# Performance work log

Measured on AMD Instinct MI355X. Metric: run time of the kernel, lower is better.

## Reference

```python
import jax, jax.numpy as jnp
import numpy as np

WINDOW = 5
PAD = WINDOW // 2


def _extract_patches(x):
    # x: (B,C,H,W) -> patches (B,C,K*K,H,W) with reflect padding, matching
    # F.pad(mode='reflect') + F.unfold(window, padding=0).
    B, C, H, W = x.shape
    xp = jnp.pad(x, ((0, 0), (0, 0), (PAD, PAD), (PAD, PAD)), mode='reflect')
    patches = jnp.stack(
        [xp[:, :, i:i + H, j:j + W] for i in range(WINDOW) for j in range(WINDOW)],
        axis=2,
    )
    return patches


def setup_inputs() -> dict:
    key = jax.random.key(0)
    k1, k2, k3 = jax.random.split(key, 3)
    x = jax.random.normal(k1, (4, 32, 256, 256), dtype=jnp.float32)
    mix = jax.random.normal(k2, (1, 32, 1, 1), dtype=jnp.float32)
    beta_raw = jax.random.normal(k3, (), dtype=jnp.float32)
    return {"x": x, "mix": mix, "beta_raw": beta_raw}


def reference(x, mix, beta_raw):
    patches = _extract_patches(x)  # (B,C,25,H,W)

    # Max filter (= max_pool2d over reflect-padded input, stride 1)
    max_out = jnp.max(patches, axis=2)

    # Soft (differentiable) median filter
    beta = 5.0 + 45.0 * jax.nn.sigmoid(beta_raw)
    center = jnp.mean(patches, axis=2, keepdims=True)
    weights = jax.nn.softmax(-beta * jnp.abs(patches - center), axis=2)
    median_out = jnp.sum(weights * patches, axis=2)

    lambda_c = jax.nn.sigmoid(mix)  # (1,C,1,1)
    return lambda_c * median_out + (1.0 - lambda_c) * max_out
```

## Files before the change

### kernel.cpp

```cpp
#include <hip/hip_runtime.h>
#include <math.h>

#define HW 256
#define TW 64
#define TH 16
#define LW 68
#define LH 20

__device__ __forceinline__ int reflect_idx(int i) {
    i = (i < 0) ? -i : i;
    i = (i >= HW) ? (2 * HW - 2 - i) : i;
    return i;
}

__device__ __forceinline__ float4 max4(float4 a, float4 b) {
    float4 r; r.x = fmaxf(a.x, b.x); r.y = fmaxf(a.y, b.y);
    r.z = fmaxf(a.z, b.z); r.w = fmaxf(a.w, b.w); return r;
}
__device__ __forceinline__ float4 max34(float4 a, float4 b, float4 c) {
    float4 r; r.x = fmaxf(fmaxf(a.x, b.x), c.x); r.y = fmaxf(fmaxf(a.y, b.y), c.y);
    r.z = fmaxf(fmaxf(a.z, b.z), c.z); r.w = fmaxf(fmaxf(a.w, b.w), c.w); return r;
}
__device__ __forceinline__ float4 add4(float4 a, float4 b) {
    float4 r; r.x = a.x + b.x; r.y = a.y + b.y;
    r.z = a.z + b.z; r.w = a.w + b.w; return r;
}

__global__ __launch_bounds__(256, 4)
void maxmedian_kernel(const float* __restrict__ x,
                      const float* __restrict__ mix,
                      const float* __restrict__ beta_raw,
                      float* __restrict__ out,
                      int C) {
    __shared__ __align__(16) float tile[LH * LW];

    const int tiles_x = HW / TW;
    const int tiles_per_plane = tiles_x * (HW / TH);
    const int plane = blockIdx.x / tiles_per_plane;
    const int t     = blockIdx.x % tiles_per_plane;
    const int ty0 = (t / tiles_x) * TH;
    const int tx0 = (t % tiles_x) * TW;

    const float* __restrict__ xp = x + (size_t)plane * (HW * HW);
    const int tid = threadIdx.x;

    {
        const int c   = tid & 63;
        const int r0s = tid >> 6;
        const int gx  = tx0 + c;
        #pragma unroll
        for (int k = 0; k < 5; ++k) {
            const int r  = r0s + 4 * k;
            const int gy = reflect_idx(ty0 + r - 2);
            tile[r * LW + c + 2] = xp[gy * HW + gx];
        }
        if (tid < 80) {
            const int jj = tid & 3;
            const int j  = (jj < 2) ? jj : (64 + jj);
            const int r  = tid >> 2;
            const int gx2 = reflect_idx(tx0 + j - 2);
            const int gy2 = reflect_idx(ty0 + r - 2);
            tile[r * LW + j] = xp[gy2 * HW + gx2];
        }
    }
    __syncthreads();

    const int ch = plane % C;
    const float lam  = 1.0f / (1.0f + __expf(-mix[ch]));
    const float beta = 5.0f + 45.0f / (1.0f + __expf(-beta_raw[0]));
    const float bp     = beta * 1.44269504088896f;
    const float inv_bp = 1.0f / bp;
    const float c04b   = 0.04f * bp;

    const int tx = tid & 15;
    const int ry = tid >> 4;
    const float* lbase = &tile[ry * LW + 4 * tx];

    const float4 w0a = *(const float4*)(lbase + 0 * LW);
    const float4 w0b = *(const float4*)(lbase + 0 * LW + 4);
    const float4 w1a = *(const float4*)(lbase + 1 * LW);
    const float4 w1b = *(const float4*)(lbase + 1 * LW + 4);
    const float4 w2a = *(const float4*)(lbase + 2 * LW);
    const float4 w2b = *(const float4*)(lbase + 2 * LW + 4);
    const float4 w3a = *(const float4*)(lbase + 3 * LW);
    const float4 w3b = *(const float4*)(lbase + 3 * LW + 4);
    const float4 w4a = *(const float4*)(lbase + 4 * LW);
    const float4 w4b = *(const float4*)(lbase + 4 * LW + 4);

    const float4 csA = add4(add4(add4(w0a, w1a), add4(w2a, w3a)), w4a);
    const float4 csB = add4(add4(add4(w0b, w1b), add4(w2b, w3b)), w4b);
    const float4 cmA = max4(max34(w0a, w1a, w2a), max4(w3a, w4a));
    const float4 cmB = max4(max34(w0b, w1b, w2b), max4(w3b, w4b));

    const float cs[8] = {csA.x,csA.y,csA.z,csA.w, csB.x,csB.y,csB.z,csB.w};
    const float cm[8] = {cmA.x,cmA.y,cmA.z,cmA.w, cmB.x,cmB.y,cmB.z,cmB.w};
    const float vv[5][8] = {
        {w0a.x,w0a.y,w0a.z,w0a.w, w0b.x,w0b.y,w0b.z,w0b.w},
        {w1a.x,w1a.y,w1a.z,w1a.w, w1b.x,w1b.y,w1b.z,w1b.w},
        {w2a.x,w2a.y,w2a.z,w2a.w, w2b.x,w2b.y,w2b.z,w2b.w},
        {w3a.x,w3a.y,w3a.z,w3a.w, w3b.x,w3b.y,w3b.z,w3b.w},
        {w4a.x,w4a.y,w4a.z,w4a.w, w4b.x,w4b.y,w4b.z,w4b.w}};

    const float t12 = cs[1] + cs[2];
    const float t34 = cs[3] + cs[4];
    const float t56 = cs[5] + cs[6];
    const float u   = t12 + t34;
    const float w_  = t34 + t56;
    const float S[4] = {cs[0] + u, u + cs[5], cs[2] + w_, w_ + cs[7]};

    const float h12 = fmaxf(cm[1], cm[2]);
    const float h34 = fmaxf(cm[3], cm[4]);
    const float h56 = fmaxf(cm[5], cm[6]);
    const float m[4] = {fmaxf(fmaxf(cm[0], h12), h34),
                        fmaxf(fmaxf(h12, h34), cm[5]),
                        fmaxf(fmaxf(cm[2], h34), h56),
                        fmaxf(fmaxf(h34, h56), cm[7])};

    float bm[4], ws[4], wa[4];
    #pragma unroll
    for (int p = 0; p < 4; ++p) { bm[p] = S[p] * c04b; ws[p] = 0.0f; wa[p] = 0.0f; }

    #pragma unroll
    for (int k = 0; k < 5; ++k) {
        #pragma unroll
        for (int j = 0; j < 5; ++j) {
            #pragma unroll
            for (int p = 0; p < 4; ++p) {
                const float tv = fmaf(bp, vv[k][p + j], -bm[p]);
                const float e  = __builtin_amdgcn_exp2f(-fabsf(tv));
                ws[p] += e;
                wa[p] = fmaf(e, tv, wa[p]);
            }
        }
    }

    float o[4];
    #pragma unroll
    for (int p = 0; p < 4; ++p) {
        const float mean = S[p] * 0.04f;
        const float med  = fmaf(wa[p] * __builtin_amdgcn_rcpf(ws[p]), inv_bp, mean);
        o[p] = fmaf(lam, med - m[p], m[p]);
    }
    float4 o4; o4.x = o[0]; o4.y = o[1]; o4.z = o[2]; o4.w = o[3];

    float* __restrict__ orow =
        out + (size_t)plane * (HW * HW) + (size_t)(ty0 + ry) * HW + (tx0 + 4 * tx);
    *(float4*)orow = o4;
}

extern "C" void kernel_launch(void* const* d_in, const int* in_sizes, int n_in,
                              void* d_out, int out_size, void* d_ws, size_t ws_size,
                              hipStream_t stream) {
    const float* x        = (const float*)d_in[0];
    const float* mix      = (const float*)d_in[1];
    const float* beta_raw = (const float*)d_in[2];
    float* out            = (float*)d_out;

    const int planes = in_sizes[0] / (HW * HW);
    const int C      = in_sizes[1];
    const int tiles_per_plane = (HW / TW) * (HW / TH);
    const int grid = planes * tiles_per_plane;

    maxmedian_kernel<<<grid, 256, 0, stream>>>(x, mix, beta_raw, out, C);
}
```

Before: 43.50 us.

## Compute two output rows per thread with a taller tile

Doubles the tile height to 32 rows, so each thread now computes a 4x2 block of outputs instead of 4x1. The two rows share loaded window rows, and the second row's column sums and maxes are derived incrementally from the first. The aim is to halve the number of blocks, reduce the relative halo load overhead, and amortise shared-memory reads and setup across more outputs. The cost is higher register pressure under launch bounds of 4 blocks per CU, and fewer blocks in flight to hide the exp-heavy compute.

```diff
diff --git a/kernel.cpp b/kernel.cpp
--- a/kernel.cpp
+++ b/kernel.cpp
@@ -3,9 +3,9 @@
 
 #define HW 256
 #define TW 64
-#define TH 16
+#define TH 32
 #define LW 68
-#define LH 20
+#define LH 36
 
 __device__ __forceinline__ int reflect_idx(int i) {
     i = (i < 0) ? -i : i;
@@ -24,6 +24,10 @@
 __device__ __forceinline__ float4 add4(float4 a, float4 b) {
     float4 r; r.x = a.x + b.x; r.y = a.y + b.y;
     r.z = a.z + b.z; r.w = a.w + b.w; return r;
+}
+__device__ __forceinline__ float4 sub4(float4 a, float4 b) {
+    float4 r; r.x = a.x - b.x; r.y = a.y - b.y;
+    r.z = a.z - b.z; r.w = a.w - b.w; return r;
 }
 
 __global__ __launch_bounds__(256, 4)
@@ -49,12 +53,12 @@
         const int r0s = tid >> 6;
         const int gx  = tx0 + c;
         #pragma unroll
-        for (int k = 0; k < 5; ++k) {
+        for (int k = 0; k < 9; ++k) {
             const int r  = r0s + 4 * k;
             const int gy = reflect_idx(ty0 + r - 2);
             tile[r * LW + c + 2] = xp[gy * HW + gx];
         }
-        if (tid < 80) {
+        if (tid < 144) {
             const int jj = tid & 3;
             const int j  = (jj < 2) ? jj : (64 + jj);
             const int r  = tid >> 2;
@@ -72,9 +76,10 @@
     const float inv_bp = 1.0f / bp;
     const float c04b   = 0.04f * bp;
 
-    const int tx = tid & 15;
-    const int ry = tid >> 4;
-    const float* lbase = &tile[ry * LW + 4 * tx];
+    const int tx  = tid & 15;
+    const int ryq = tid >> 4;
+    const int r0  = ryq * 2;
+    const float* lbase = &tile[r0 * LW + 4 * tx];
 
     const float4 w0a = *(const float4*)(lbase + 0 * LW);
     const float4 w0b = *(const float4*)(lbase + 0 * LW + 4);
@@ -86,39 +91,64 @@
     const float4 w3b = *(const float4*)(lbase + 3 * LW + 4);
     const float4 w4a = *(const float4*)(lbase + 4 * LW);
     const float4 w4b = *(const float4*)(lbase + 4 * LW + 4);
-
-    const float4 csA = add4(add4(add4(w0a, w1a), add4(w2a, w3a)), w4a);
-    const float4 csB = add4(add4(add4(w0b, w1b), add4(w2b, w3b)), w4b);
-    const float4 cmA = max4(max34(w0a, w1a, w2a), max4(w3a, w4a));
-    const float4 cmB = max4(max34(w0b, w1b, w2b), max4(w3b, w4b));
-
-    const float cs[8] = {csA.x,csA.y,csA.z,csA.w, csB.x,csB.y,csB.z,csB.w};
-    const float cm[8] = {cmA.x,cmA.y,cmA.z,cmA.w, cmB.x,cmB.y,cmB.z,cmB.w};
-    const float vv[5][8] = {
+    const float4 w5a = *(const float4*)(lbase + 5 * LW);
+    const float4 w5b = *(const float4*)(lbase + 5 * LW + 4);
+
+    const float4 cs0A = add4(add4(add4(w0a, w1a), add4(w2a, w3a)), w4a);
+    const float4 cs0B = add4(add4(add4(w0b, w1b), add4(w2b, w3b)), w4b);
+    const float4 cs1A = add4(cs0A, sub4(w5a, w0a));
+    const float4 cs1B = add4(cs0B, sub4(w5b, w0b));
+
+    const float4 p12a = max4(w1a, w2a), p12b = max4(w1b, w2b);
+    const float4 p34a = max4(w3a, w4a), p34b = max4(w3b, w4b);
+    const float4 cm0A = max34(w0a, p12a, p34a);
+    const float4 cm0B = max34(w0b, p12b, p34b);
+    const float4 cm1A = max34(p12a, p34a, w5a);
+    const float4 cm1B = max34(p12b, p34b, w5b);
+
+    const float vv[6][8] = {
         {w0a.x,w0a.y,w0a.z,w0a.w, w0b.x,w0b.y,w0b.z,w0b.w},
         {w1a.x,w1a.y,w1a.z,w1a.w, w1b.x,w1b.y,w1b.z,w1b.w},
         {w2a.x,w2a.y,w2a.z,w2a.w, w2b.x,w2b.y,w2b.z,w2b.w},
         {w3a.x,w3a.y,w3a.z,w3a.w, w3b.x,w3b.y,w3b.z,w3b.w},
-        {w4a.x,w4a.y,w4a.z,w4a.w, w4b.x,w4b.y,w4b.z,w4b.w}};
-
-    const float t12 = cs[1] + cs[2];
-    const float t34 = cs[3] + cs[4];
-    const float t56 = cs[5] + cs[6];
-    const float u   = t12 + t34;
-    const float w_  = t34 + t56;
-    const float S[4] = {cs[0] + u, u + cs[5], cs[2] + w_, w_ + cs[7]};
-
-    const float h12 = fmaxf(cm[1], cm[2]);
-    const float h34 = fmaxf(cm[3], cm[4]);
-    const float h56 = fmaxf(cm[5], cm[6]);
-    const float m[4] = {fmaxf(fmaxf(cm[0], h12), h34),
-                        fmaxf(fmaxf(h12, h34), cm[5]),
-                        fmaxf(fmaxf(cm[2], h34), h56),
-                        fmaxf(fmaxf(h34, h56), cm[7])};
-
-    float bm[4], ws[4], wa[4];
+        {w4a.x,w4a.y,w4a.z,w4a.w, w4b.x,w4b.y,w4b.z,w4b.w},
+        {w5a.x,w5a.y,w5a.z,w5a.w, w5b.x,w5b.y,w5b.z,w5b.w}};
+    const float cs0[8] = {cs0A.x,cs0A.y,cs0A.z,cs0A.w, cs0B.x,cs0B.y,cs0B.z,cs0B.w};
+    const float cs1[8] = {cs1A.x,cs1A.y,cs1A.z,cs1A.w, cs1B.x,cs1B.y,cs1B.z,cs1B.w};
+    const float cm0[8] = {cm0A.x,cm0A.y,cm0A.z,cm0A.w, cm0B.x,cm0B.y,cm0B.z,cm0B.w};
+    const float cm1[8] = {cm1A.x,cm1A.y,cm1A.z,cm1A.w, cm1B.x,cm1B.y,cm1B.z,cm1B.w};
+
+    float S0[4], S1[4], m0[4], m1[4];
+    {
+        const float a12 = cs0[1] + cs0[2], a34 = cs0[3] + cs0[4], a56 = cs0[5] + cs0[6];
+        const float au = a12 + a34, aw = a34 + a56;
+        S0[0] = cs0[0] + au; S0[1] = au + cs0[5]; S0[2] = cs0[2] + aw; S0[3] = aw + cs0[7];
+        const float b12 = cs1[1] + cs1[2], b34 = cs1[3] + cs1[4], b56 = cs1[5] + cs1[6];
+        const float bu = b12 + b34, bw = b34 + b56;
+        S1[0] = cs1[0] + bu; S1[1] = bu + cs1[5]; S1[2] = cs1[2] + bw; S1[3] = bw + cs1[7];
+
+        const float h12 = fmaxf(cm0[1], cm0[2]);
+        const float h34 = fmaxf(cm0[3], cm0[4]);
+        const float h56 = fmaxf(cm0[5], cm0[6]);
+        m0[0] = fmaxf(fmaxf(cm0[0], h12), h34);
+        m0[1] = fmaxf(fmaxf(h12, h34), cm0[5]);
+        m0[2] = fmaxf(fmaxf(cm0[2], h34), h56);
+        m0[3] = fmaxf(fmaxf(h34, h56), cm0[7]);
+        const float g12 = fmaxf(cm1[1], cm1[2]);
+        const float g34 = fmaxf(cm1[3], cm1[4]);
+        const float g56 = fmaxf(cm1[5], cm1[6]);
+        m1[0] = fmaxf(fmaxf(cm1[0], g12), g34);
+        m1[1] = fmaxf(fmaxf(g12, g34), cm1[5]);
+        m1[2] = fmaxf(fmaxf(cm1[2], g34), g56);
+        m1[3] = fmaxf(fmaxf(g34, g56), cm1[7]);
+    }
+
+    float bm0[4], bm1[4], ws0[4], wa0[4], ws1[4], wa1[4];
     #pragma unroll
-    for (int p = 0; p < 4; ++p) { bm[p] = S[p] * c04b; ws[p] = 0.0f; wa[p] = 0.0f; }
+    for (int p = 0; p < 4; ++p) {
+        bm0[p] = S0[p] * c04b; ws0[p] = 0.0f; wa0[p] = 0.0f;
+        bm1[p] = S1[p] * c04b; ws1[p] = 0.0f; wa1[p] = 0.0f;
+    }
 
     #pragma unroll
     for (int k = 0; k < 5; ++k) {
@@ -126,26 +156,38 @@
         for (int j = 0; j < 5; ++j) {
             #pragma unroll
             for (int p = 0; p < 4; ++p) {
-                const float tv = fmaf(bp, vv[k][p + j], -bm[p]);
-                const float e  = __builtin_amdgcn_exp2f(-fabsf(tv));
-                ws[p] += e;
-                wa[p] = fmaf(e, tv, wa[p]);
+                const float v0  = vv[k][p + j];
+                const float tv0 = fmaf(bp, v0, -bm0[p]);
+                const float e0  = __builtin_amdgcn_exp2f(-fabsf(tv0));
+                ws0[p] += e0;
+                wa0[p] = fmaf(e0, tv0, wa0[p]);
+
+                const float v1  = vv[k + 1][p + j];
+                const float tv1 = fmaf(bp, v1, -bm1[p]);
+                const float e1  = __builtin_amdgcn_exp2f(-fabsf(tv1));
+                ws1[p] += e1;
+                wa1[p] = fmaf(e1, tv1, wa1[p]);
             }
         }
     }
 
-    float o[4];
+    float* __restrict__ orow =
+        out + (size_t)plane * (HW * HW) + (size_t)(ty0 + r0) * HW + (tx0 + 4 * tx);
+
+    float o0[4], o1[4];
     #pragma unroll
     for (int p = 0; p < 4; ++p) {
-        const float mean = S[p] * 0.04f;
-        const float med  = fmaf(wa[p] * __builtin_amdgcn_rcpf(ws[p]), inv_bp, mean);
-        o[p] = fmaf(lam, med - m[p], m[p]);
-    }
-    float4 o4; o4.x = o[0]; o4.y = o[1]; o4.z = o[2]; o4.w = o[3];
-
-    float* __restrict__ orow =
-        out + (size_t)plane * (HW * HW) + (size_t)(ty0 + ry) * HW + (tx0 + 4 * tx);
-    *(float4*)orow = o4;
+        const float mean0 = S0[p] * 0.04f;
+        const float med0  = fmaf(wa0[p] * __builtin_amdgcn_rcpf(ws0[p]), inv_bp, mean0);
+        o0[p] = fmaf(lam, med0 - m0[p], m0[p]);
+        const float mean1 = S1[p] * 0.04f;
+        const float med1  = fmaf(wa1[p] * __builtin_amdgcn_rcpf(ws1[p]), inv_bp, mean1);
+        o1[p] = fmaf(lam, med1 - m1[p], m1[p]);
+    }
+    float4 q0; q0.x = o0[0]; q0.y = o0[1]; q0.z = o0[2]; q0.w = o0[3];
+    float4 q1; q1.x = o1[0]; q1.y = o1[1]; q1.z = o1[2]; q1.w = o1[3];
+    *(float4*)orow = q0;
+    *(float4*)(orow + HW) = q1;
 }
 
 extern "C" void kernel_launch(void* const* d_in, const int* in_sizes, int n_in,
```

After: 39.48 us. 9.2% less time.
